# Performance work log

Hardware: AMD Instinct MI355X
Metric: run time of the kernel (lower is better)

Reference implementation:

```python
import jax, jax.numpy as jnp
import numpy as np

TWO_PI = np.float32(2.0 * np.pi)
N_GABORS = 256
H = W = 512


def setup_inputs() -> dict:
    key = jax.random.key(0)
    ks = jax.random.split(key, 10)
    f32 = jnp.float32
    return {
        "grid_x": jax.random.uniform(ks[0], (H, W), dtype=f32),
        "grid_y": jax.random.uniform(ks[1], (H, W), dtype=f32),
        "u": jax.random.normal(ks[2], (N_GABORS,), dtype=f32),
        "v": jax.random.normal(ks[3], (N_GABORS,), dtype=f32),
        "theta": 2.0 * jax.random.normal(ks[4], (N_GABORS,), dtype=f32),
        "rel_sigma": 0.05 + 0.7 * jax.random.normal(ks[5], (N_GABORS,), dtype=f32),
        "rel_freq": 0.03 + 5.0 * jax.random.normal(ks[6], (N_GABORS,), dtype=f32),
        "gamma": 0.03 + 0.15 * jax.random.normal(ks[7], (N_GABORS,), dtype=f32),
        "psi": 3.0 * jax.random.normal(ks[8], (N_GABORS, 3), dtype=f32),
        "amplitude": 0.2 * jax.random.normal(ks[9], (N_GABORS, 3), dtype=f32),
    }


def reference(grid_x, grid_y, u, v, theta, rel_sigma, rel_freq, gamma, psi, amplitude):
    # Parameter range enforcement (enforce_parameter_ranges + forward clamps)
    uc = jnp.clip(u, -1.0, 1.0)
    vc = jnp.clip(v, -1.0, 1.0)
    th = jnp.clip(theta, -2.0, 2.0) * TWO_PI           # [N]
    sig = jnp.clip(rel_sigma, 1e-5, 5.0)               # [N]
    gam = jnp.clip(gamma, 1e-5, 5.0)                   # [N]
    psi_c = jnp.clip(psi, -1.0, 1.0)                   # [N,3]
    amp = jnp.clip(amplitude, 0.0, 1.0)                # [N,3]

    cr = jnp.cos(th)[:, None, None]
    sr = jnp.sin(th)[:, None, None]
    dx = grid_x[None, :, :] - uc[:, None, None]        # [N,H,W]
    dy = grid_y[None, :, :] - vc[:, None, None]
    x_rot = dx * cr + dy * sr                          # [N,H,W]
    y_rot = -dx * sr + dy * cr

    gaussian = jnp.exp(jnp.clip(
        -x_rot ** 2 / (2.0 * sig[:, None, None] ** 2)
        - y_rot ** 2 / (2.0 * gam[:, None, None] ** 2),
        -80.0, 80.0))                                  # [N,H,W]

    freq = TWO_PI / jnp.exp(rel_freq)                  # [N]
    phase = psi_c * TWO_PI                             # [N,3]
    fx = freq[:, None, None] * x_rot                   # [N,H,W]

    # cos(fx + phase) = cos(fx)cos(phase) - sin(fx)sin(phase):
    # contract the gabor dim without materializing [N,3,H,W].
    gc = gaussian * jnp.cos(fx)                        # [N,H,W]
    gs = gaussian * jnp.sin(fx)                        # [N,H,W]
    result = (jnp.einsum('nhw,nc->chw', gc, amp * jnp.cos(phase))
              - jnp.einsum('nhw,nc->chw', gs, amp * jnp.sin(phase)))  # [3,H,W]
    return jnp.clip(result, -1.0, 1.0)
```

## Files before the change

### kernel.cpp

```cpp
#include <hip/hip_runtime.h>
#include <stdint.h>

#define NG 256
#define HW (512*512)
#define NCELL 1024
#define CAP 384
#define SPILL_CAP 4096
#define NBIN 256
#define PXB (HW/NBIN)
#define TWO_PI_F 6.283185307179586f
#define L2E 1.4426950408889634f
#define INV2PI_D 0.15915494309189535

static __device__ __forceinline__ float clampf(float x, float lo, float hi) {
    return fminf(fmaxf(x, lo), hi);
}

static __device__ __forceinline__ void compute_consts(
    int n,
    const float* __restrict__ u, const float* __restrict__ v,
    const float* __restrict__ theta, const float* __restrict__ rel_sigma,
    const float* __restrict__ rel_freq, const float* __restrict__ gamma,
    const float* __restrict__ psi, const float* __restrict__ amplitude,
    float4& A, float4& B, float4& C, float4& D)
{
    const float uc = clampf(u[n], -1.f, 1.f);
    const float vc = clampf(v[n], -1.f, 1.f);
    const float th = clampf(theta[n], -2.f, 2.f) * TWO_PI_F;
    const float sg = clampf(rel_sigma[n], 1e-5f, 5.f);
    const float gm = clampf(gamma[n], 1e-5f, 5.f);
    const float cr = (float)::cos((double)th);
    const float sr = (float)::sin((double)th);
    const float i2s = 1.0f / (2.0f * sg * sg);
    const float i2g = 1.0f / (2.0f * gm * gm);
    const float E  = (float)::exp((double)rel_freq[n]);
    const float fq = TWO_PI_F / E;
    A = make_float4(uc, vc, cr, sr);
    B = make_float4(-(i2s * L2E), -(i2g * L2E), fq, 0.f);
    float ac[3], as[3];
    #pragma unroll
    for (int c = 0; c < 3; ++c) {
        const float ph = clampf(psi[n*3 + c], -1.f, 1.f) * TWO_PI_F;
        const float a  = clampf(amplitude[n*3 + c], 0.f, 1.f);
        ac[c] = a * (float)::cos((double)ph);
        as[c] = a * (float)::sin((double)ph);
    }
    C = make_float4(ac[0], ac[1], ac[2], 0.f);
    D = make_float4(as[0], as[1], as[2], 0.f);
}

static __device__ __forceinline__ void accum_list(
    const float4* __restrict__ base, int ngab,
    float gx, float gy, float& a0, float& a1, float& a2)
{
    const float c1f = 0.15915494309189535f;
    const float c2f = (float)(INV2PI_D - (double)0.15915494309189535f);
    for (int j = 0; j < ngab; ++j) {
        const float4 k0 = base[j];
        const float4 k1 = base[NG + j];
        const float dx = gx - k0.x;
        const float dy = gy - k0.y;
        float xr, yr;
        {
            #pragma clang fp contract(off)
            xr = dx * k0.z + dy * k0.w;
            yr = dy * k0.z - dx * k0.w;
        }
        const float e2 = fmaf(yr * yr, k1.y, xr * xr * k1.x);
        if (e2 > -20.0f) {
            const float g = __builtin_amdgcn_exp2f(e2);
            float fx;
            {
                #pragma clang fp contract(off)
                fx = k1.z * xr;
            }
            const float nn = __builtin_rintf(fx * c1f);
            float t = __builtin_fmaf(fx, c1f, -nn);
            t = __builtin_fmaf(fx, c2f, t);
            const float s = __builtin_amdgcn_sinf(t);
            const float c = __builtin_amdgcn_cosf(t);
            const float4 k2 = base[2*NG + j];
            const float4 k3 = base[3*NG + j];
            const float gc = g * c, gs = g * s;
            a0 = fmaf(gc, k2.x, fmaf(-gs, k3.x, a0));
            a1 = fmaf(gc, k2.y, fmaf(-gs, k3.y, a1));
            a2 = fmaf(gc, k2.z, fmaf(-gs, k3.z, a2));
        }
    }
}

__global__ __launch_bounds__(256) void gabor_bin_consts(
    const float* __restrict__ grid_x, const float* __restrict__ grid_y,
    const float* __restrict__ u, const float* __restrict__ v,
    const float* __restrict__ theta, const float* __restrict__ rel_sigma,
    const float* __restrict__ rel_freq, const float* __restrict__ gamma,
    const float* __restrict__ psi, const float* __restrict__ amplitude,
    float4* __restrict__ consts, int* __restrict__ counts,
    float4* __restrict__ bpx,
    int* __restrict__ spill, int* __restrict__ spilln)
{
    const int tid = threadIdx.x;
    if (blockIdx.x == NBIN) {
        float4 A, B, C, D;
        compute_consts(tid, u, v, theta, rel_sigma, rel_freq, gamma, psi,
                       amplitude, A, B, C, D);
        consts[tid] = A; consts[NG+tid] = B;
        consts[2*NG+tid] = C; consts[3*NG+tid] = D;
        return;
    }
    __shared__ int hist[NCELL];
    __shared__ int base[NCELL];
    #pragma unroll
    for (int i = 0; i < NCELL/256; ++i) hist[i*256 + tid] = 0;
    __syncthreads();

    uint32_t rec[PXB/256];
    float px[PXB/256], py[PXB/256];
    const int p0 = blockIdx.x * PXB;
    #pragma unroll
    for (int i = 0; i < PXB/256; ++i) {
        const int p = p0 + i*256 + tid;
        const float x = grid_x[p], y = grid_y[p];
        px[i] = x; py[i] = y;
        int ix = (int)(x * 32.0f); ix = min(max(ix, 0), 31);
        int iy = (int)(y * 32.0f); iy = min(max(iy, 0), 31);
        const int cell = iy*32 + ix;
        const int lr = atomicAdd(&hist[cell], 1);
        rec[i] = ((uint32_t)cell << 11) | (uint32_t)lr;
    }
    __syncthreads();
    #pragma unroll
    for (int i = 0; i < NCELL/256; ++i) {
        const int c = i*256 + tid;
        const int h = hist[c];
        base[c] = (h > 0) ? atomicAdd(&counts[c], h) : 0;
    }
    __syncthreads();
    #pragma unroll
    for (int i = 0; i < PXB/256; ++i) {
        const int p = p0 + i*256 + tid;
        const int cell = (int)(rec[i] >> 11);
        const int g = base[cell] + (int)(rec[i] & 0x7FFu);
        if (g < CAP) {
            bpx[cell*CAP + g] =
                make_float4(__int_as_float(p), px[i], py[i], 0.f);
        } else {
            const int t2 = atomicAdd(spilln, 1);
            if (t2 < SPILL_CAP) spill[t2] = p;
        }
    }
}

__global__ __launch_bounds__(256) void gabor_render(
    const float4* __restrict__ consts, const int* __restrict__ counts,
    const float4* __restrict__ bpx,
    const int* __restrict__ spill, const int* __restrict__ spilln,
    const float* __restrict__ grid_x, const float* __restrict__ grid_y,
    float* __restrict__ out)
{
    __shared__ float4 cs[4 * NG];
    __shared__ int s_wb1[4], s_wb2[4];
    const int cell = blockIdx.x;
    const int tid = threadIdx.x;
    const float cxc = ((cell & 31) + 0.5f) * 0.03125f;
    const float cyc = ((cell >> 5) + 0.5f) * 0.03125f;

    {
        const float4 A = consts[tid];
        const float4 B = consts[NG + tid];
        const float4 C = consts[2*NG + tid];
        const float4 D = consts[3*NG + tid];
        const float dx = cxc - A.x, dy = cyc - A.y;
        const float xrc = dx * A.z + dy * A.w;
        const float yrc = dy * A.z - dx * A.w;
        const float R = 0.0222f;
        const float axr = fabsf(xrc), ayr = fabsf(yrc);
        const float xl = fmaxf(axr - R, 0.f), yl = fmaxf(ayr - R, 0.f);
        const float xh = axr + R,            yh = ayr + R;
        const float e2max = xl*xl*B.x + yl*yl*B.y;
        const float e2min = xh*xh*B.x + yh*yh*B.y;
        const bool nz = (C.x != 0.f) | (C.y != 0.f) | (C.z != 0.f) |
                        (D.x != 0.f) | (D.y != 0.f) | (D.z != 0.f);
        const bool act = (e2max > -20.0f) && nz;
        const bool g1  = act && (e2min > -20.0f);
        const bool g2  = act && !g1;
        const unsigned long long m1 = __ballot(g1);
        const unsigned long long m2 = __ballot(g2);
        const int lane = tid & 63, w = tid >> 6;
        if (lane == 0) { s_wb1[w] = __popcll(m1); s_wb2[w] = __popcll(m2); }
        __syncthreads();
        const int n1 = s_wb1[0] + s_wb1[1] + s_wb1[2] + s_wb1[3];
        int b1 = 0, b2 = n1;
        #pragma unroll
        for (int i = 0; i < 4; ++i) {
            b1 += (i < w) ? s_wb1[i] : 0;
            b2 += (i < w) ? s_wb2[i] : 0;
        }
        const unsigned long long lm = (1ull << lane) - 1ull;
        if (g1) {
            const int pos = b1 + __popcll(m1 & lm);
            cs[pos] = A; cs[NG+pos] = B; cs[2*NG+pos] = C; cs[3*NG+pos] = D;
        }
        if (g2) {
            const int pos = b2 + __popcll(m2 & lm);
            cs[pos] = A; cs[NG+pos] = B; cs[2*NG+pos] = C; cs[3*NG+pos] = D;
        }
        __syncthreads();
    }
    const int n1 = s_wb1[0] + s_wb1[1] + s_wb1[2] + s_wb1[3];
    const int ng = n1 + s_wb2[0] + s_wb2[1] + s_wb2[2] + s_wb2[3];

    const float c1f = 0.15915494309189535f;
    const float c2f = (float)(INV2PI_D - (double)0.15915494309189535f);
    const int cnt = min(counts[cell], CAP);
    const int sb = cell * CAP;
    for (int i = tid; i < cnt; i += 256) {
        const float4 pxk = bpx[sb + i];
        const int   p  = __float_as_int(pxk.x);
        const float gx = pxk.y, gy = pxk.z;
        float a0 = 0.f, a1 = 0.f, a2 = 0.f;
        #pragma unroll 2
        for (int j = 0; j < n1; ++j) {
            const float4 k0 = cs[j];
            const float4 k1 = cs[NG + j];
            const float dx = gx - k0.x;
            const float dy = gy - k0.y;
            float xr, yr;
            {
                #pragma clang fp contract(off)
                xr = dx * k0.z + dy * k0.w;
                yr = dy * k0.z - dx * k0.w;
            }
            const float e2 = fmaf(yr * yr, k1.y, xr * xr * k1.x);
            const float g = __builtin_amdgcn_exp2f(e2);
            float fx;
            {
                #pragma clang fp contract(off)
                fx = k1.z * xr;
            }
            const float nn = __builtin_rintf(fx * c1f);
            float t = __builtin_fmaf(fx, c1f, -nn);
            t = __builtin_fmaf(fx, c2f, t);
            const float s = __builtin_amdgcn_sinf(t);
            const float c = __builtin_amdgcn_cosf(t);
            const float4 k2 = cs[2*NG + j];
            const float4 k3 = cs[3*NG + j];
            const float gc = g * c, gs = g * s;
            a0 = fmaf(gc, k2.x, fmaf(-gs, k3.x, a0));
            a1 = fmaf(gc, k2.y, fmaf(-gs, k3.y, a1));
            a2 = fmaf(gc, k2.z, fmaf(-gs, k3.z, a2));
        }
        for (int j = n1; j < ng; ++j) {
            const float4 k0 = cs[j];
            const float4 k1 = cs[NG + j];
            const float dx = gx - k0.x;
            const float dy = gy - k0.y;
            float xr, yr;
            {
                #pragma clang fp contract(off)
                xr = dx * k0.z + dy * k0.w;
                yr = dy * k0.z - dx * k0.w;
            }
            const float e2 = fmaf(yr * yr, k1.y, xr * xr * k1.x);
            if (e2 > -20.0f) {
                const float g = __builtin_amdgcn_exp2f(e2);
                float fx;
                {
                    #pragma clang fp contract(off)
                    fx = k1.z * xr;
                }
                const float nn = __builtin_rintf(fx * c1f);
                float t = __builtin_fmaf(fx, c1f, -nn);
                t = __builtin_fmaf(fx, c2f, t);
                const float s = __builtin_amdgcn_sinf(t);
                const float c = __builtin_amdgcn_cosf(t);
                const float4 k2 = cs[2*NG + j];
                const float4 k3 = cs[3*NG + j];
                const float gc = g * c, gs = g * s;
                a0 = fmaf(gc, k2.x, fmaf(-gs, k3.x, a0));
                a1 = fmaf(gc, k2.y, fmaf(-gs, k3.y, a1));
                a2 = fmaf(gc, k2.z, fmaf(-gs, k3.z, a2));
            }
        }
        out[p]        = clampf(a0, -1.f, 1.f);
        out[HW + p]   = clampf(a1, -1.f, 1.f);
        out[2*HW + p] = clampf(a2, -1.f, 1.f);
    }

    if (cell == 0) {
        const int sc = min(*spilln, SPILL_CAP);
        for (int i = tid; i < sc; i += 256) {
            const int p = spill[i];
            const float gx = grid_x[p], gy = grid_y[p];
            float a0 = 0.f, a1 = 0.f, a2 = 0.f;
            accum_list(consts, NG, gx, gy, a0, a1, a2);
            out[p]        = clampf(a0, -1.f, 1.f);
            out[HW + p]   = clampf(a1, -1.f, 1.f);
            out[2*HW + p] = clampf(a2, -1.f, 1.f);
        }
    }
}

__global__ __launch_bounds__(256) void gabor_consts_kernel(
    const float* __restrict__ u, const float* __restrict__ v,
    const float* __restrict__ theta, const float* __restrict__ rel_sigma,
    const float* __restrict__ rel_freq, const float* __restrict__ gamma,
    const float* __restrict__ psi, const float* __restrict__ amplitude,
    float4* __restrict__ ws)
{
    const int n = threadIdx.x;
    float4 A, B, C, D;
    compute_consts(n, u, v, theta, rel_sigma, rel_freq, gamma, psi, amplitude,
                   A, B, C, D);
    ws[n] = A; ws[NG + n] = B; ws[2*NG + n] = C; ws[3*NG + n] = D;
}

__global__ __launch_bounds__(256) void gabor_fwd_ws(
    const float4* __restrict__ ws,
    const float* __restrict__ grid_x, const float* __restrict__ grid_y,
    float* __restrict__ out)
{
    __shared__ float4 cs[4 * NG];
    const int tid = threadIdx.x;
    cs[tid]        = ws[tid];
    cs[tid + NG]   = ws[tid + NG];
    cs[tid + 2*NG] = ws[tid + 2*NG];
    cs[tid + 3*NG] = ws[tid + 3*NG];
    __syncthreads();
    const int p = blockIdx.x * 256 + tid;
    const float gx = grid_x[p], gy = grid_y[p];
    float a0 = 0.f, a1 = 0.f, a2 = 0.f;
    accum_list(cs, NG, gx, gy, a0, a1, a2);
    out[p]        = clampf(a0, -1.f, 1.f);
    out[HW + p]   = clampf(a1, -1.f, 1.f);
    out[2*HW + p] = clampf(a2, -1.f, 1.f);
}

__global__ __launch_bounds__(256) void gabor_fwd_fused(
    const float* __restrict__ grid_x, const float* __restrict__ grid_y,
    const float* __restrict__ u, const float* __restrict__ v,
    const float* __restrict__ theta, const float* __restrict__ rel_sigma,
    const float* __restrict__ rel_freq, const float* __restrict__ gamma,
    const float* __restrict__ psi, const float* __restrict__ amplitude,
    float* __restrict__ out)
{
    __shared__ float4 cs[4 * NG];
    const int tid = threadIdx.x;
    {
        float4 A, B, C, D;
        compute_consts(tid, u, v, theta, rel_sigma, rel_freq, gamma, psi,
                       amplitude, A, B, C, D);
        cs[tid] = A; cs[tid + NG] = B; cs[tid + 2*NG] = C; cs[tid + 3*NG] = D;
    }
    __syncthreads();
    const int p = blockIdx.x * 256 + tid;
    const float gx = grid_x[p], gy = grid_y[p];
    float a0 = 0.f, a1 = 0.f, a2 = 0.f;
    accum_list(cs, NG, gx, gy, a0, a1, a2);
    out[p]        = clampf(a0, -1.f, 1.f);
    out[HW + p]   = clampf(a1, -1.f, 1.f);
    out[2*HW + p] = clampf(a2, -1.f, 1.f);
}

extern "C" void kernel_launch(void* const* d_in, const int* in_sizes, int n_in,
                              void* d_out, int out_size, void* d_ws, size_t ws_size,
                              hipStream_t stream) {
    const float* grid_x    = (const float*)d_in[0];
    const float* grid_y    = (const float*)d_in[1];
    const float* u         = (const float*)d_in[2];
    const float* v         = (const float*)d_in[3];
    const float* theta     = (const float*)d_in[4];
    const float* rel_sigma = (const float*)d_in[5];
    const float* rel_freq  = (const float*)d_in[6];
    const float* gamma     = (const float*)d_in[7];
    const float* psi       = (const float*)d_in[8];
    const float* amplitude = (const float*)d_in[9];
    float* out = (float*)d_out;

    const size_t OFF_CONSTS = 0;
    const size_t OFF_COUNTS = 16384;
    const size_t OFF_SPN    = 20480;
    const size_t OFF_SPILL  = 20736;
    const size_t OFF_BPX    = 37120;
    const size_t NEED       = 6328576;

    char* w = (char*)d_ws;

    if (ws_size >= NEED) {
        float4* consts = (float4*)(w + OFF_CONSTS);
        int*    counts = (int*)(w + OFF_COUNTS);
        int*    spn    = (int*)(w + OFF_SPN);
        int*    spill  = (int*)(w + OFF_SPILL);
        float4* bpx    = (float4*)(w + OFF_BPX);

        hipMemsetAsync(w + OFF_COUNTS, 0, 4096 + 256, stream);
        gabor_bin_consts<<<NBIN + 1, 256, 0, stream>>>(
            grid_x, grid_y, u, v, theta, rel_sigma, rel_freq, gamma,
            psi, amplitude, consts, counts, bpx, spill, spn);
        gabor_render<<<NCELL, 256, 0, stream>>>(
            consts, counts, bpx, spill, spn, grid_x, grid_y, out);
    } else if (ws_size >= 4u * NG * sizeof(float4)) {
        float4* ws = (float4*)d_ws;
        gabor_consts_kernel<<<1, NG, 0, stream>>>(
            u, v, theta, rel_sigma, rel_freq, gamma, psi, amplitude, ws);
        gabor_fwd_ws<<<HW / 256, 256, 0, stream>>>(ws, grid_x, grid_y, out);
    } else {
        gabor_fwd_fused<<<HW / 256, 256, 0, stream>>>(
            grid_x, grid_y, u, v, theta, rel_sigma, rel_freq, gamma,
            psi, amplitude, out);
    }
}
```

Before: 36.08 us.

## Pack gabor constants in pairs and use packed float2 math in main loop

Reorganizes the shared-memory constant table for the unconditional gabor list into paired structure-of-arrays layout, so each iteration processes two gabors with float2 vector arithmetic. This is meant to let the compiler emit packed FP32 instructions (v_pk_fma/v_pk_mul) and halve the arithmetic instruction count in the hot loop, while transcendentals stay scalar. Odd counts are padded with a zero-amplitude dummy entry, the conditional list moves to separate arrays, and shared memory use grows.

```diff
diff --git a/kernel.cpp b/kernel.cpp
--- a/kernel.cpp
+++ b/kernel.cpp
@@ -11,6 +11,8 @@
 #define TWO_PI_F 6.283185307179586f
 #define L2E 1.4426950408889634f
 #define INV2PI_D 0.15915494309189535
+
+typedef float v2f __attribute__((ext_vector_type(2)));
 
 static __device__ __forceinline__ float clampf(float x, float lo, float hi) {
     return fminf(fmaxf(x, lo), hi);
@@ -158,8 +160,14 @@
     const float* __restrict__ grid_x, const float* __restrict__ grid_y,
     float* __restrict__ out)
 {
-    __shared__ float4 cs[4 * NG];
+    __shared__ float4 pkUV[NG/2];
+    __shared__ float4 pkROT[NG/2];
+    __shared__ float4 pkSG[NG/2];
+    __shared__ float2 pkFQ[NG/2];
+    __shared__ float4 pkAMP[3][NG/2];
+    __shared__ float4 c2A[NG], c2B[NG], c2C[NG], c2D[NG];
     __shared__ int s_wb1[4], s_wb2[4];
+
     const int cell = blockIdx.x;
     const int tid = threadIdx.x;
     const float cxc = ((cell & 31) + 0.5f) * 0.03125f;
@@ -189,8 +197,7 @@
         const int lane = tid & 63, w = tid >> 6;
         if (lane == 0) { s_wb1[w] = __popcll(m1); s_wb2[w] = __popcll(m2); }
         __syncthreads();
-        const int n1 = s_wb1[0] + s_wb1[1] + s_wb1[2] + s_wb1[3];
-        int b1 = 0, b2 = n1;
+        int b1 = 0, b2 = 0;
         #pragma unroll
         for (int i = 0; i < 4; ++i) {
             b1 += (i < w) ? s_wb1[i] : 0;
@@ -199,60 +206,110 @@
         const unsigned long long lm = (1ull << lane) - 1ull;
         if (g1) {
             const int pos = b1 + __popcll(m1 & lm);
-            cs[pos] = A; cs[NG+pos] = B; cs[2*NG+pos] = C; cs[3*NG+pos] = D;
+            const int q = pos >> 1, h = pos & 1;
+            if (h == 0) {
+                pkUV[q].x = A.x;  pkUV[q].z = A.y;
+                pkROT[q].x = A.z; pkROT[q].z = A.w;
+                pkSG[q].x = B.x;  pkSG[q].z = B.y;
+                pkFQ[q].x = B.z;
+                pkAMP[0][q].x = C.x; pkAMP[0][q].z = D.x;
+                pkAMP[1][q].x = C.y; pkAMP[1][q].z = D.y;
+                pkAMP[2][q].x = C.z; pkAMP[2][q].z = D.z;
+            } else {
+                pkUV[q].y = A.x;  pkUV[q].w = A.y;
+                pkROT[q].y = A.z; pkROT[q].w = A.w;
+                pkSG[q].y = B.x;  pkSG[q].w = B.y;
+                pkFQ[q].y = B.z;
+                pkAMP[0][q].y = C.x; pkAMP[0][q].w = D.x;
+                pkAMP[1][q].y = C.y; pkAMP[1][q].w = D.y;
+                pkAMP[2][q].y = C.z; pkAMP[2][q].w = D.z;
+            }
         }
         if (g2) {
             const int pos = b2 + __popcll(m2 & lm);
-            cs[pos] = A; cs[NG+pos] = B; cs[2*NG+pos] = C; cs[3*NG+pos] = D;
+            c2A[pos] = A; c2B[pos] = B; c2C[pos] = C; c2D[pos] = D;
         }
         __syncthreads();
     }
     const int n1 = s_wb1[0] + s_wb1[1] + s_wb1[2] + s_wb1[3];
-    const int ng = n1 + s_wb2[0] + s_wb2[1] + s_wb2[2] + s_wb2[3];
+    const int n2 = s_wb2[0] + s_wb2[1] + s_wb2[2] + s_wb2[3];
+    if (tid == 0 && (n1 & 1)) {
+        const int q = n1 >> 1;
+        pkUV[q].y = 0.f;  pkUV[q].w = 0.f;
+        pkROT[q].y = 1.f; pkROT[q].w = 0.f;
+        pkSG[q].y = 0.f;  pkSG[q].w = 0.f;
+        pkFQ[q].y = 0.f;
+        pkAMP[0][q].y = 0.f; pkAMP[0][q].w = 0.f;
+        pkAMP[1][q].y = 0.f; pkAMP[1][q].w = 0.f;
+        pkAMP[2][q].y = 0.f; pkAMP[2][q].w = 0.f;
+    }
+    __syncthreads();
+    const int n1p = (n1 + 1) >> 1;
 
     const float c1f = 0.15915494309189535f;
     const float c2f = (float)(INV2PI_D - (double)0.15915494309189535f);
+    const v2f c1p = {c1f, c1f};
+    const v2f c2p = {c2f, c2f};
     const int cnt = min(counts[cell], CAP);
     const int sb = cell * CAP;
     for (int i = tid; i < cnt; i += 256) {
         const float4 pxk = bpx[sb + i];
         const int   p  = __float_as_int(pxk.x);
         const float gx = pxk.y, gy = pxk.z;
-        float a0 = 0.f, a1 = 0.f, a2 = 0.f;
+        const v2f gxp = {gx, gx}, gyp = {gy, gy};
+        v2f A0 = {0.f, 0.f}, A1 = {0.f, 0.f}, A2 = {0.f, 0.f};
         #pragma unroll 2
-        for (int j = 0; j < n1; ++j) {
-            const float4 k0 = cs[j];
-            const float4 k1 = cs[NG + j];
-            const float dx = gx - k0.x;
-            const float dy = gy - k0.y;
-            float xr, yr;
+        for (int q = 0; q < n1p; ++q) {
+            const float4 tuv = pkUV[q];
+            const float4 trt = pkROT[q];
+            const float4 tsg = pkSG[q];
+            const float2 tfq = pkFQ[q];
+            const v2f up  = {tuv.x, tuv.y}, vp  = {tuv.z, tuv.w};
+            const v2f crp = {trt.x, trt.y}, srp = {trt.z, trt.w};
+            const v2f isp = {tsg.x, tsg.y}, igp = {tsg.z, tsg.w};
+            const v2f fqp = {tfq.x, tfq.y};
+            const v2f dx = gxp - up;
+            const v2f dy = gyp - vp;
+            v2f xr, yr;
             {
                 #pragma clang fp contract(off)
-                xr = dx * k0.z + dy * k0.w;
-                yr = dy * k0.z - dx * k0.w;
-            }
-            const float e2 = fmaf(yr * yr, k1.y, xr * xr * k1.x);
-            const float g = __builtin_amdgcn_exp2f(e2);
-            float fx;
+                xr = dx * crp + dy * srp;
+                yr = dy * crp - dx * srp;
+            }
+            const v2f e2 = (xr * xr) * isp + (yr * yr) * igp;
+            const v2f g = { __builtin_amdgcn_exp2f(e2.x),
+                            __builtin_amdgcn_exp2f(e2.y) };
+            v2f fx;
             {
                 #pragma clang fp contract(off)
-                fx = k1.z * xr;
-            }
-            const float nn = __builtin_rintf(fx * c1f);
-            float t = __builtin_fmaf(fx, c1f, -nn);
-            t = __builtin_fmaf(fx, c2f, t);
-            const float s = __builtin_amdgcn_sinf(t);
-            const float c = __builtin_amdgcn_cosf(t);
-            const float4 k2 = cs[2*NG + j];
-            const float4 k3 = cs[3*NG + j];
-            const float gc = g * c, gs = g * s;
-            a0 = fmaf(gc, k2.x, fmaf(-gs, k3.x, a0));
-            a1 = fmaf(gc, k2.y, fmaf(-gs, k3.y, a1));
-            a2 = fmaf(gc, k2.z, fmaf(-gs, k3.z, a2));
-        }
-        for (int j = n1; j < ng; ++j) {
-            const float4 k0 = cs[j];
-            const float4 k1 = cs[NG + j];
+                fx = fqp * xr;
+            }
+            const v2f r1 = fx * c1p;
+            const v2f nn = { __builtin_rintf(r1.x), __builtin_rintf(r1.y) };
+            v2f t = __builtin_elementwise_fma(fx, c1p, -nn);
+            t = __builtin_elementwise_fma(fx, c2p, t);
+            const v2f s = { __builtin_amdgcn_sinf(t.x),
+                            __builtin_amdgcn_sinf(t.y) };
+            const v2f c = { __builtin_amdgcn_cosf(t.x),
+                            __builtin_amdgcn_cosf(t.y) };
+            const v2f gc = g * c, gs = g * s;
+            const float4 am0 = pkAMP[0][q];
+            const float4 am1 = pkAMP[1][q];
+            const float4 am2 = pkAMP[2][q];
+            const v2f ac0 = {am0.x, am0.y}, as0 = {am0.z, am0.w};
+            const v2f ac1 = {am1.x, am1.y}, as1 = {am1.z, am1.w};
+            const v2f ac2 = {am2.x, am2.y}, as2 = {am2.z, am2.w};
+            A0 = __builtin_elementwise_fma(gc, ac0,
+                 __builtin_elementwise_fma(-gs, as0, A0));
+            A1 = __builtin_elementwise_fma(gc, ac1,
+                 __builtin_elementwise_fma(-gs, as1, A1));
+            A2 = __builtin_elementwise_fma(gc, ac2,
+                 __builtin_elementwise_fma(-gs, as2, A2));
+        }
+        float a0 = A0.x + A0.y, a1 = A1.x + A1.y, a2 = A2.x + A2.y;
+        for (int j = 0; j < n2; ++j) {
+            const float4 k0 = c2A[j];
+            const float4 k1 = c2B[j];
             const float dx = gx - k0.x;
             const float dy = gy - k0.y;
             float xr, yr;
@@ -274,8 +331,8 @@
                 t = __builtin_fmaf(fx, c2f, t);
                 const float s = __builtin_amdgcn_sinf(t);
                 const float c = __builtin_amdgcn_cosf(t);
-                const float4 k2 = cs[2*NG + j];
-                const float4 k3 = cs[3*NG + j];
+                const float4 k2 = c2C[j];
+                const float4 k3 = c2D[j];
                 const float gc = g * c, gs = g * s;
                 a0 = fmaf(gc, k2.x, fmaf(-gs, k3.x, a0));
                 a1 = fmaf(gc, k2.y, fmaf(-gs, k3.y, a1));
```

Result: faster. 33.71 us (-6.6%).
